# Performance work log

Measured on AMD Instinct MI355X. Metric: run time of the kernel, lower is better.

## Reference

```python
import jax, jax.numpy as jnp
import numpy as np

N = 50000      # number of nodes in batch
K = 32         # padded max neighbors
D = 100        # emb_dim
V = 500000     # n_items
LAYERS = 2


def setup_inputs() -> dict:
    key = jax.random.key(0)
    ks = jax.random.split(key, 9)
    nodes = jax.random.randint(ks[0], (N,), 0, V)
    nei = jax.random.randint(ks[1], (N, K), 0, V)          # padded neighbor ids (pad = 0)
    wei = jax.random.uniform(ks[2], (N, K), dtype=jnp.float32)  # edge weights (pad = 0 in real data)
    s_vec = jax.random.normal(ks[3], (N, D), dtype=jnp.float32)
    emb = jax.random.normal(ks[4], (V, D), dtype=jnp.float32) * 0.02
    emb = emb.at[0].set(0.0)                               # padding_idx=0
    W1_w = jax.random.normal(ks[5], (D + 1, D), dtype=jnp.float32) / np.sqrt(D + 1).astype(np.float32)
    W1_b = jnp.zeros((D,), dtype=jnp.float32)
    q1_w = jax.random.normal(ks[6], (D,), dtype=jnp.float32) / np.sqrt(D).astype(np.float32)
    W2_w = jax.random.normal(ks[7], (2 * D, D), dtype=jnp.float32) / np.sqrt(2 * D).astype(np.float32)
    W2_b = jnp.zeros((D,), dtype=jnp.float32)
    return {"nodes": nodes, "nei": nei, "wei": wei, "s_vec": s_vec,
            "emb": emb, "W1_w": W1_w, "W1_b": W1_b, "q1_w": q1_w,
            "W2_w": W2_w, "W2_b": W2_b}


def reference(nodes, nei, wei, s_vec, emb, W1_w, W1_b, q1_w, W2_w, W2_b):
    # x: [N, D] embeddings of the batch nodes
    x = emb[nodes]
    # In the torch code nei/wei are rebuilt identically every layer and h_nei always
    # comes from the frozen embedding table, so the attention message `msg` is
    # layer-invariant; compute it once (same math as the original loop).
    h_nei = emb[nei]                                              # [N, K, D]
    feat = jnp.concatenate([h_nei * s_vec[:, None, :], wei[..., None]], axis=-1)  # [N, K, D+1]
    score = jnp.einsum('nkd,d->nk', jnp.tanh(feat @ W1_w + W1_b), q1_w)           # [N, K]
    att = jax.nn.softmax(score, axis=-1)                          # no masking, as in original
    msg = jnp.einsum('nk,nkd->nd', att, h_nei)                    # [N, D]
    for _ in range(LAYERS):
        x = jax.nn.relu(jnp.concatenate([x, msg], axis=-1) @ W2_w + W2_b)
    return x
```

## Files before the change

### kernel.cpp

```cpp
#include <hip/hip_runtime.h>
#include <cstdint>
#include <cstddef>

typedef __attribute__((ext_vector_type(8))) short bf16x8;
typedef __attribute__((ext_vector_type(16))) float f32x16;

__device__ __forceinline__ unsigned short f2bf(float f) {
    unsigned int u = __builtin_bit_cast(unsigned int, f);
    u += 0x7fffu + ((u >> 16) & 1u);
    return (unsigned short)(u >> 16);
}

__device__ __forceinline__ unsigned int pk2(float a, float b) {
#if __has_builtin(__builtin_amdgcn_cvt_pk_bf16_f32)
    auto r = __builtin_amdgcn_cvt_pk_bf16_f32(a, b);
    return __builtin_bit_cast(unsigned int, r);
#else
    return (unsigned int)f2bf(a) | ((unsigned int)f2bf(b) << 16);
#endif
}

template<int CTRL>
__device__ __forceinline__ float dpp_add(float v) {
    int t = __builtin_amdgcn_update_dpp(0, __builtin_bit_cast(int, v), CTRL, 0xf, 0xf, true);
    return v + __builtin_bit_cast(float, t);
}

__device__ __forceinline__ float swz16_add(float v) {
    int t = __builtin_amdgcn_ds_swizzle(__builtin_bit_cast(int, v), 0x401F);
    return v + __builtin_bit_cast(float, t);
}

__device__ __forceinline__ float fast_tanh(float x) {
    float e = __expf(2.0f * x);
    return 1.0f - 2.0f / (e + 1.0f);
}

__global__ void prep_kernel(const float* __restrict__ W1, const float* __restrict__ W2,
                            unsigned short* __restrict__ W1t, unsigned short* __restrict__ W2t)
{
    int idx = blockIdx.x * 256 + threadIdx.x;
    if (idx < 128 * 128) {
        int nn = idx >> 7, kk = idx & 127;
        W1t[idx] = (nn < 100 && kk < 100) ? f2bf(W1[kk * 100 + nn]) : (unsigned short)0;
    } else {
        int j = idx - 128 * 128;
        if (j < 128 * 208) {
            int nn = j / 208, kk = j - nn * 208;
            unsigned short v = 0;
            if (nn < 100) {
                if (kk < 100) v = f2bf(W2[kk * 100 + nn]);
                else if (kk >= 104 && kk < 204) v = f2bf(W2[(kk - 4) * 100 + nn]);
            }
            W2t[j] = v;
        }
    }
}

#define HP 104

__global__ __launch_bounds__(256) void fused_kernel(
    const int* __restrict__ nodes, const int* __restrict__ nei,
    const float* __restrict__ wei, const float* __restrict__ s_vec,
    const float* __restrict__ emb, const float* __restrict__ W1,
    const float* __restrict__ b1, const float* __restrict__ q1,
    const unsigned short* __restrict__ W1t, const unsigned short* __restrict__ W2t,
    const float* __restrict__ b2, float* __restrict__ out, int N)
{
    __shared__ __align__(16) unsigned short h_s[32 * HP];
    __shared__ __align__(16) unsigned short hst[14 * 32 * 8];
    __shared__ __align__(16) unsigned short msg_s[32 * HP];
    __shared__ __align__(16) float part2[4 * 100];
    __shared__ __align__(16) float spart[128];
    __shared__ __align__(16) float wei_s[32];

    const int tid  = threadIdx.x;
    const int lane = tid & 63;
    const int w    = tid >> 6;
    const int col  = lane & 31;
    const int hi   = lane >> 5;
    const int n    = w * 32 + col;
    const int n0   = blockIdx.x * 32;

    bf16x8 Bf1[7];
    #pragma unroll
    for (int ks = 0; ks < 7; ++ks)
        Bf1[ks] = *(const bf16x8*)(W1t + n * 128 + ks * 16 + hi * 8);

    float b1r[16], w100r[16], q1r[16];
    #pragma unroll
    for (int r = 0; r < 16; ++r) {
        int nn = w * 32 + (r & 3) + 8 * (r >> 2) + 4 * hi;
        bool ok = nn < 100;
        b1r[r]   = ok ? b1[nn] : 0.0f;
        w100r[r] = ok ? W1[100 * 100 + nn] : 0.0f;
        q1r[r]   = ok ? q1[nn] : 0.0f;
    }
    const bool nok = (n < 100);

    if (tid < 32) {
        *(uint2*)&hst[(12 * 32 + tid) * 8 + 4] = make_uint2(0, 0);
        *(uint4*)&hst[(13 * 32 + tid) * 8]     = make_uint4(0, 0, 0, 0);
        *(uint2*)&h_s[tid * HP + 100]          = make_uint2(0, 0);
        *(uint2*)&msg_s[tid * HP + 100]        = make_uint2(0, 0);
    }

    const int gk = tid >> 3;
    const int gj = tid & 7;
    const bool t24 = (gj == 0);

    float4 h0, h1, h2, h3, s0, s1, s2, s3;
    int   nidx_pf = 0;
    float wv = 0.0f;
    {
        int nid0 = nei[(size_t)n0 * 32 + gk];
        const float4* erow = (const float4*)(emb + (size_t)nid0 * 100);
        const float4* srow = (const float4*)(s_vec + (size_t)n0 * 100);
        h0 = erow[gj];      s0 = srow[gj];
        h1 = erow[gj + 8];  s1 = srow[gj + 8];
        h2 = erow[gj + 16]; s2 = srow[gj + 16];
        if (t24) { h3 = erow[24]; s3 = srow[24]; }
        if (tid < 32) wv = wei[(size_t)n0 * 32 + tid];
        if (n0 + 1 < N) nidx_pf = nei[(size_t)(n0 + 1) * 32 + gk];
    }
    __syncthreads();

    for (int it = 0; it < 32; ++it) {
        const int node = n0 + it;
        if (node >= N) break;

        if (tid < 32) wei_s[tid] = wv;
        {
            #define ST_C4(c4, h4, s4) { \
                *(uint2*)&h_s[gk * HP + (c4) * 4] = \
                    make_uint2(pk2(h4.x, h4.y), pk2(h4.z, h4.w)); \
                *(uint2*)&hst[(((c4) >> 1) * 32 + gk) * 8 + ((c4) & 1) * 4] = \
                    make_uint2(pk2(h4.x * s4.x, h4.y * s4.y), pk2(h4.z * s4.z, h4.w * s4.w)); }
            ST_C4(gj,      h0, s0)
            ST_C4(gj + 8,  h1, s1)
            ST_C4(gj + 16, h2, s2)
            if (t24) { ST_C4(24, h3, s3) }
            #undef ST_C4
        }
        if (it + 1 < 32 && node + 1 < N) {
            const float4* erow = (const float4*)(emb + (size_t)nidx_pf * 100);
            const float4* srow = (const float4*)(s_vec + (size_t)(node + 1) * 100);
            h0 = erow[gj];      s0 = srow[gj];
            h1 = erow[gj + 8];  s1 = srow[gj + 8];
            h2 = erow[gj + 16]; s2 = srow[gj + 16];
            if (t24) { h3 = erow[24]; s3 = srow[24]; }
            if (tid < 32) wv = wei[(size_t)(node + 1) * 32 + tid];
            if (it + 2 < 32 && node + 2 < N) nidx_pf = nei[(size_t)(node + 2) * 32 + gk];
        }
        __syncthreads();

        const float wk = wei_s[col];
        f32x16 acc;
        #pragma unroll
        for (int r = 0; r < 16; ++r) acc[r] = fmaf(wk, w100r[r], b1r[r]);
        #pragma unroll
        for (int ks = 0; ks < 7; ++ks) {
            bf16x8 hfrag = *(const bf16x8*)&hst[((2 * ks + hi) * 32 + col) * 8];
            acc = __builtin_amdgcn_mfma_f32_32x32x16_bf16(Bf1[ks], hfrag, acc, 0, 0, 0);
        }

        float part = 0.0f;
        #pragma unroll
        for (int r = 0; r < 16; ++r) part = fmaf(fast_tanh(acc[r]), q1r[r], part);
        part += __shfl_xor(part, 32);
        if (lane < 32) spart[w * 32 + lane] = part;
        __syncthreads();

        float attk;
        {
            float s = spart[col] + spart[32 + col] + spart[64 + col] + spart[96 + col];
            float mx = s;
            #pragma unroll
            for (int off = 16; off; off >>= 1) mx = fmaxf(mx, __shfl_xor(mx, off));
            float e = __expf(s - mx);
            float den = e;
            #pragma unroll
            for (int off = 16; off; off >>= 1) den += __shfl_xor(den, off);
            float attv = e / den;
            attk = __shfl(attv, w * 8 + (lane >> 3));
        }

        {
            const int oct  = lane & 7;
            const int krow = w * 8 + (lane >> 3);
            const float a  = attk;
            uint4 r1 = *(const uint4*)&h_s[krow * HP + oct * 8];
            const int oct2 = (oct < 5) ? oct : 4;
            uint4 r2 = *(const uint4*)&h_s[krow * HP + 64 + oct2 * 8];
            float m1[8], m2[8];
            #define UNP2(u, d0, d1) { d0 = __builtin_bit_cast(float, (u) << 16); \
                                      d1 = __builtin_bit_cast(float, (u) & 0xffff0000u); }
            { float t0,t1; UNP2(r1.x,t0,t1); m1[0]=a*t0; m1[1]=a*t1; }
            { float t0,t1; UNP2(r1.y,t0,t1); m1[2]=a*t0; m1[3]=a*t1; }
            { float t0,t1; UNP2(r1.z,t0,t1); m1[4]=a*t0; m1[5]=a*t1; }
            { float t0,t1; UNP2(r1.w,t0,t1); m1[6]=a*t0; m1[7]=a*t1; }
            { float t0,t1; UNP2(r2.x,t0,t1); m2[0]=a*t0; m2[1]=a*t1; }
            { float t0,t1; UNP2(r2.y,t0,t1); m2[2]=a*t0; m2[3]=a*t1; }
            { float t0,t1; UNP2(r2.z,t0,t1); m2[4]=a*t0; m2[5]=a*t1; }
            { float t0,t1; UNP2(r2.w,t0,t1); m2[6]=a*t0; m2[7]=a*t1; }
            #undef UNP2
            #pragma unroll
            for (int j = 0; j < 8; ++j) {
                m1[j] = dpp_add<0x128>(m1[j]);
                m2[j] = dpp_add<0x128>(m2[j]);
            }
            #pragma unroll
            for (int j = 0; j < 8; ++j) {
                m1[j] = swz16_add(m1[j]);
                m2[j] = swz16_add(m2[j]);
            }
            #pragma unroll
            for (int j = 0; j < 8; ++j) {
                m1[j] += __shfl_xor(m1[j], 32);
                m2[j] += __shfl_xor(m2[j], 32);
            }
            if ((lane >> 3) == 0) {
                float* p = &part2[w * 100];
                *(float4*)&p[oct * 8]     = make_float4(m1[0], m1[1], m1[2], m1[3]);
                *(float4*)&p[oct * 8 + 4] = make_float4(m1[4], m1[5], m1[6], m1[7]);
                if (oct < 5) *(float4*)&p[64 + oct * 8]     = make_float4(m2[0], m2[1], m2[2], m2[3]);
                if (oct < 4) *(float4*)&p[64 + oct * 8 + 4] = make_float4(m2[4], m2[5], m2[6], m2[7]);
            }
        }
        __syncthreads();

        if (w < 2) {
            int d = w * 64 + lane;
            if (d < 100) {
                float s = part2[d] + part2[100 + d] + part2[200 + d] + part2[300 + d];
                msg_s[it * HP + d] = f2bf(s);
            }
        }
    }

    __syncthreads();

    bf16x8 Bf2[13];
    #pragma unroll
    for (int ks = 0; ks < 13; ++ks)
        Bf2[ks] = *(const bf16x8*)(W2t + n * 208 + ks * 16 + hi * 8);
    const float b2v = nok ? b2[n] : 0.0f;
    {
        int row = n0 + gk;
        int rc = row < N ? row : N - 1;
        const float4* xr = (const float4*)(emb + (size_t)nodes[rc] * 100);
        float4 x0 = xr[gj], x1 = xr[gj + 8], x2 = xr[gj + 16];
        float4 x3;
        if (t24) x3 = xr[24];
        *(uint2*)&h_s[gk * HP + gj * 4]        = make_uint2(pk2(x0.x, x0.y), pk2(x0.z, x0.w));
        *(uint2*)&h_s[gk * HP + (gj + 8) * 4]  = make_uint2(pk2(x1.x, x1.y), pk2(x1.z, x1.w));
        *(uint2*)&h_s[gk * HP + (gj + 16) * 4] = make_uint2(pk2(x2.x, x2.y), pk2(x2.z, x2.w));
        if (t24)
            *(uint2*)&h_s[gk * HP + 96]        = make_uint2(pk2(x3.x, x3.y), pk2(x3.z, x3.w));
    }
    __syncthreads();

    #define AFRAG(ks) (*(const bf16x8*)( \
        (ks) < 6  ? &h_s[col * HP + (ks) * 16 + hi * 8] : \
        (ks) == 6 ? (hi ? &msg_s[col * HP] : &h_s[col * HP + 96]) : \
                    &msg_s[col * HP + (ks) * 16 + hi * 8 - 104]))

    f32x16 acc;
    #pragma unroll
    for (int r = 0; r < 16; ++r) acc[r] = b2v;
    #pragma unroll
    for (int ks = 0; ks < 13; ++ks)
        acc = __builtin_amdgcn_mfma_f32_32x32x16_bf16(AFRAG(ks), Bf2[ks], acc, 0, 0, 0);
    __syncthreads();
    if (nok) {
        #pragma unroll
        for (int r = 0; r < 16; ++r) {
            int m = (r & 3) + 8 * (r >> 2) + 4 * hi;
            h_s[m * HP + n] = f2bf(fmaxf(acc[r], 0.0f));
        }
    }
    __syncthreads();

    f32x16 acc2;
    #pragma unroll
    for (int r = 0; r < 16; ++r) acc2[r] = b2v;
    #pragma unroll
    for (int ks = 0; ks < 13; ++ks)
        acc2 = __builtin_amdgcn_mfma_f32_32x32x16_bf16(AFRAG(ks), Bf2[ks], acc2, 0, 0, 0);
    #undef AFRAG
    if (nok) {
        #pragma unroll
        for (int r = 0; r < 16; ++r) {
            int m = (r & 3) + 8 * (r >> 2) + 4 * hi;
            int row = n0 + m;
            if (row < N) out[(size_t)row * 100 + n] = fmaxf(acc2[r], 0.0f);
        }
    }
}

extern "C" void kernel_launch(void* const* d_in, const int* in_sizes, int n_in,
                              void* d_out, int out_size, void* d_ws, size_t ws_size,
                              hipStream_t stream) {
    const int*   nodes = (const int*)d_in[0];
    const int*   nei   = (const int*)d_in[1];
    const float* wei   = (const float*)d_in[2];
    const float* s_vec = (const float*)d_in[3];
    const float* emb   = (const float*)d_in[4];
    const float* W1    = (const float*)d_in[5];
    const float* b1    = (const float*)d_in[6];
    const float* q1    = (const float*)d_in[7];
    const float* W2    = (const float*)d_in[8];
    const float* b2    = (const float*)d_in[9];
    float* out = (float*)d_out;
    const int N = in_sizes[0];

    unsigned short* W1t = (unsigned short*)d_ws;
    unsigned short* W2t = W1t + 128 * 128;

    prep_kernel<<<168, 256, 0, stream>>>(W1, W2, W1t, W2t);
    const int gB = (N + 31) / 32;
    fused_kernel<<<gB, 256, 0, stream>>>(nodes, nei, wei, s_vec, emb, W1, b1, q1,
                                         W1t, W2t, b2, out, N);
}
```

Before: 641.4 us.

## Cut register pressure: fold wei and bias into MFMA, pack q1, drop s prefetch

Adds the edge weight and the W1 bias as extra K columns of the first MFMA by writing wei and a constant 1 into the padded LDS tile, which removes the per-lane bias and W1 row-100 registers. q1 is packed into bf16 pairs, the s_vec prefetch registers are dropped in favour of loading s_vec in the current iteration, and W2 fragments are read from global memory at use instead of being held in registers. Launch bounds now request 7 waves per SIMD to raise occupancy. In exchange, s_vec loads are no longer hidden behind the previous iteration, bias, weight and q1 pick up bf16 rounding, and the W2 reads may add latency.

```diff
diff --git a/kernel.cpp b/kernel.cpp
--- a/kernel.cpp
+++ b/kernel.cpp
@@ -36,13 +36,20 @@
     return 1.0f - 2.0f / (e + 1.0f);
 }
 
-__global__ void prep_kernel(const float* __restrict__ W1, const float* __restrict__ W2,
+__global__ void prep_kernel(const float* __restrict__ W1, const float* __restrict__ b1,
+                            const float* __restrict__ W2,
                             unsigned short* __restrict__ W1t, unsigned short* __restrict__ W2t)
 {
     int idx = blockIdx.x * 256 + threadIdx.x;
     if (idx < 128 * 128) {
         int nn = idx >> 7, kk = idx & 127;
-        W1t[idx] = (nn < 100 && kk < 100) ? f2bf(W1[kk * 100 + nn]) : (unsigned short)0;
+        unsigned short v = 0;
+        if (nn < 100) {
+            if (kk < 100)       v = f2bf(W1[kk * 100 + nn]);
+            else if (kk == 100) v = f2bf(W1[100 * 100 + nn]);
+            else if (kk == 101) v = f2bf(b1[nn]);
+        }
+        W1t[idx] = v;
     } else {
         int j = idx - 128 * 128;
         if (j < 128 * 208) {
@@ -59,11 +66,10 @@
 
 #define HP 104
 
-__global__ __launch_bounds__(256) void fused_kernel(
+__global__ __launch_bounds__(256, 7) void fused_kernel(
     const int* __restrict__ nodes, const int* __restrict__ nei,
     const float* __restrict__ wei, const float* __restrict__ s_vec,
-    const float* __restrict__ emb, const float* __restrict__ W1,
-    const float* __restrict__ b1, const float* __restrict__ q1,
+    const float* __restrict__ emb, const float* __restrict__ q1,
     const unsigned short* __restrict__ W1t, const unsigned short* __restrict__ W2t,
     const float* __restrict__ b2, float* __restrict__ out, int N)
 {
@@ -72,7 +78,6 @@
     __shared__ __align__(16) unsigned short msg_s[32 * HP];
     __shared__ __align__(16) float part2[4 * 100];
     __shared__ __align__(16) float spart[128];
-    __shared__ __align__(16) float wei_s[32];
 
     const int tid  = threadIdx.x;
     const int lane = tid & 63;
@@ -87,39 +92,37 @@
     for (int ks = 0; ks < 7; ++ks)
         Bf1[ks] = *(const bf16x8*)(W1t + n * 128 + ks * 16 + hi * 8);
 
-    float b1r[16], w100r[16], q1r[16];
-    #pragma unroll
-    for (int r = 0; r < 16; ++r) {
-        int nn = w * 32 + (r & 3) + 8 * (r >> 2) + 4 * hi;
-        bool ok = nn < 100;
-        b1r[r]   = ok ? b1[nn] : 0.0f;
-        w100r[r] = ok ? W1[100 * 100 + nn] : 0.0f;
-        q1r[r]   = ok ? q1[nn] : 0.0f;
+    unsigned int q1p[8];
+    #pragma unroll
+    for (int j = 0; j < 8; ++j) {
+        int r  = 2 * j;
+        int nj = w * 32 + (r & 3) + 8 * (r >> 2) + 4 * hi;
+        float a = (nj     < 100) ? q1[nj]     : 0.0f;
+        float b = (nj + 1 < 100) ? q1[nj + 1] : 0.0f;
+        q1p[j] = pk2(a, b);
     }
     const bool nok = (n < 100);
 
     if (tid < 32) {
-        *(uint2*)&hst[(12 * 32 + tid) * 8 + 4] = make_uint2(0, 0);
-        *(uint4*)&hst[(13 * 32 + tid) * 8]     = make_uint4(0, 0, 0, 0);
-        *(uint2*)&h_s[tid * HP + 100]          = make_uint2(0, 0);
-        *(uint2*)&msg_s[tid * HP + 100]        = make_uint2(0, 0);
+        *(uint4*)&hst[(13 * 32 + tid) * 8] = make_uint4(0, 0, 0, 0);
+        *(uint2*)&h_s[tid * HP + 100]      = make_uint2(0, 0);
+        *(uint2*)&msg_s[tid * HP + 100]    = make_uint2(0, 0);
     }
 
     const int gk = tid >> 3;
     const int gj = tid & 7;
     const bool t24 = (gj == 0);
 
-    float4 h0, h1, h2, h3, s0, s1, s2, s3;
+    float4 h0, h1, h2, h3;
     int   nidx_pf = 0;
     float wv = 0.0f;
     {
         int nid0 = nei[(size_t)n0 * 32 + gk];
         const float4* erow = (const float4*)(emb + (size_t)nid0 * 100);
-        const float4* srow = (const float4*)(s_vec + (size_t)n0 * 100);
-        h0 = erow[gj];      s0 = srow[gj];
-        h1 = erow[gj + 8];  s1 = srow[gj + 8];
-        h2 = erow[gj + 16]; s2 = srow[gj + 16];
-        if (t24) { h3 = erow[24]; s3 = srow[24]; }
+        h0 = erow[gj];
+        h1 = erow[gj + 8];
+        h2 = erow[gj + 16];
+        if (t24) h3 = erow[24];
         if (tid < 32) wv = wei[(size_t)n0 * 32 + tid];
         if (n0 + 1 < N) nidx_pf = nei[(size_t)(n0 + 1) * 32 + gk];
     }
@@ -129,35 +132,38 @@
         const int node = n0 + it;
         if (node >= N) break;
 
-        if (tid < 32) wei_s[tid] = wv;
+        if (tid < 32)
+            *(uint2*)&hst[(12 * 32 + tid) * 8 + 4] = make_uint2(pk2(wv, 1.0f), 0u);
         {
+            const float4* srow = (const float4*)(s_vec + (size_t)node * 100);
+            float4 sA = srow[gj], sB = srow[gj + 8], sC = srow[gj + 16];
+            float4 sD;
+            if (t24) sD = srow[24];
             #define ST_C4(c4, h4, s4) { \
                 *(uint2*)&h_s[gk * HP + (c4) * 4] = \
                     make_uint2(pk2(h4.x, h4.y), pk2(h4.z, h4.w)); \
                 *(uint2*)&hst[(((c4) >> 1) * 32 + gk) * 8 + ((c4) & 1) * 4] = \
                     make_uint2(pk2(h4.x * s4.x, h4.y * s4.y), pk2(h4.z * s4.z, h4.w * s4.w)); }
-            ST_C4(gj,      h0, s0)
-            ST_C4(gj + 8,  h1, s1)
-            ST_C4(gj + 16, h2, s2)
-            if (t24) { ST_C4(24, h3, s3) }
+            ST_C4(gj,      h0, sA)
+            ST_C4(gj + 8,  h1, sB)
+            ST_C4(gj + 16, h2, sC)
+            if (t24) { ST_C4(24, h3, sD) }
             #undef ST_C4
         }
         if (it + 1 < 32 && node + 1 < N) {
             const float4* erow = (const float4*)(emb + (size_t)nidx_pf * 100);
-            const float4* srow = (const float4*)(s_vec + (size_t)(node + 1) * 100);
-            h0 = erow[gj];      s0 = srow[gj];
-            h1 = erow[gj + 8];  s1 = srow[gj + 8];
-            h2 = erow[gj + 16]; s2 = srow[gj + 16];
-            if (t24) { h3 = erow[24]; s3 = srow[24]; }
+            h0 = erow[gj];
+            h1 = erow[gj + 8];
+            h2 = erow[gj + 16];
+            if (t24) h3 = erow[24];
             if (tid < 32) wv = wei[(size_t)(node + 1) * 32 + tid];
             if (it + 2 < 32 && node + 2 < N) nidx_pf = nei[(size_t)(node + 2) * 32 + gk];
         }
         __syncthreads();
 
-        const float wk = wei_s[col];
         f32x16 acc;
         #pragma unroll
-        for (int r = 0; r < 16; ++r) acc[r] = fmaf(wk, w100r[r], b1r[r]);
+        for (int r = 0; r < 16; ++r) acc[r] = 0.0f;
         #pragma unroll
         for (int ks = 0; ks < 7; ++ks) {
             bf16x8 hfrag = *(const bf16x8*)&hst[((2 * ks + hi) * 32 + col) * 8];
@@ -166,7 +172,12 @@
 
         float part = 0.0f;
         #pragma unroll
-        for (int r = 0; r < 16; ++r) part = fmaf(fast_tanh(acc[r]), q1r[r], part);
+        for (int j = 0; j < 8; ++j) {
+            float qa = __builtin_bit_cast(float, q1p[j] << 16);
+            float qb = __builtin_bit_cast(float, q1p[j] & 0xffff0000u);
+            part = fmaf(fast_tanh(acc[2 * j]),     qa, part);
+            part = fmaf(fast_tanh(acc[2 * j + 1]), qb, part);
+        }
         part += __shfl_xor(part, 32);
         if (lane < 32) spart[w * 32 + lane] = part;
         __syncthreads();
@@ -240,10 +251,6 @@
 
     __syncthreads();
 
-    bf16x8 Bf2[13];
-    #pragma unroll
-    for (int ks = 0; ks < 13; ++ks)
-        Bf2[ks] = *(const bf16x8*)(W2t + n * 208 + ks * 16 + hi * 8);
     const float b2v = nok ? b2[n] : 0.0f;
     {
         int row = n0 + gk;
@@ -264,13 +271,14 @@
         (ks) < 6  ? &h_s[col * HP + (ks) * 16 + hi * 8] : \
         (ks) == 6 ? (hi ? &msg_s[col * HP] : &h_s[col * HP + 96]) : \
                     &msg_s[col * HP + (ks) * 16 + hi * 8 - 104]))
+    #define BFRAG(ks) (*(const bf16x8*)(W2t + n * 208 + (ks) * 16 + hi * 8))
 
     f32x16 acc;
     #pragma unroll
     for (int r = 0; r < 16; ++r) acc[r] = b2v;
     #pragma unroll
     for (int ks = 0; ks < 13; ++ks)
-        acc = __builtin_amdgcn_mfma_f32_32x32x16_bf16(AFRAG(ks), Bf2[ks], acc, 0, 0, 0);
+        acc = __builtin_amdgcn_mfma_f32_32x32x16_bf16(AFRAG(ks), BFRAG(ks), acc, 0, 0, 0);
     __syncthreads();
     if (nok) {
         #pragma unroll
@@ -286,8 +294,9 @@
     for (int r = 0; r < 16; ++r) acc2[r] = b2v;
     #pragma unroll
     for (int ks = 0; ks < 13; ++ks)
-        acc2 = __builtin_amdgcn_mfma_f32_32x32x16_bf16(AFRAG(ks), Bf2[ks], acc2, 0, 0, 0);
+        acc2 = __builtin_amdgcn_mfma_f32_32x32x16_bf16(AFRAG(ks), BFRAG(ks), acc2, 0, 0, 0);
     #undef AFRAG
+    #undef BFRAG
     if (nok) {
         #pragma unroll
         for (int r = 0; r < 16; ++r) {
@@ -317,8 +326,8 @@
     unsigned short* W1t = (unsigned short*)d_ws;
     unsigned short* W2t = W1t + 128 * 128;
 
-    prep_kernel<<<168, 256, 0, stream>>>(W1, W2, W1t, W2t);
+    prep_kernel<<<168, 256, 0, stream>>>(W1, b1, W2, W1t, W2t);
     const int gB = (N + 31) / 32;
-    fused_kernel<<<gB, 256, 0, stream>>>(nodes, nei, wei, s_vec, emb, W1, b1, q1,
+    fused_kernel<<<gB, 256, 0, stream>>>(nodes, nei, wei, s_vec, emb, q1,
                                          W1t, W2t, b2, out, N);
 }
```

Measured after the change: 865.8 us. +35.0%, slower.
